# Performance work log

Measured on AMD Instinct MI355X. Metric: run time of the kernel, lower is better.

The kernel has to match this reference:

```python
import jax, jax.numpy as jnp
import numpy as np

N_NODES = 50000
N_EDGES = 800000
T = 3          # number of graph snapshots
L = 2          # num_layers
D = 128        # node feat dim == hidden dim
DE = 16        # edge feat dim


def setup_inputs() -> dict:
    key = jax.random.key(0)
    ks = jax.random.split(key, 12)
    return {
        "src": jax.random.randint(ks[0], (T, N_EDGES), 0, N_NODES, dtype=jnp.int32),
        "dst": jax.random.randint(ks[1], (T, N_EDGES), 0, N_NODES, dtype=jnp.int32),
        "n_feats": jax.random.normal(ks[2], (T, N_NODES, D), dtype=jnp.float32),
        "e_feats": jax.random.normal(ks[3], (T, N_EDGES, DE), dtype=jnp.float32),
        "W0": jax.random.normal(ks[4], (L, D, D), dtype=jnp.float32) * (1.0 / np.sqrt(D)),
        "lstm_Wih": jax.random.normal(ks[5], (L, 4 * D, D), dtype=jnp.float32) * (1.0 / np.sqrt(D)),
        "lstm_Whh": jax.random.normal(ks[6], (L, 4 * D, D), dtype=jnp.float32) * (1.0 / np.sqrt(D)),
        "lstm_bih": jnp.zeros((L, 4 * D), dtype=jnp.float32),
        "lstm_bhh": jnp.zeros((L, 4 * D), dtype=jnp.float32),
        "a_w": jax.random.normal(ks[7], (L, 2 * D + DE), dtype=jnp.float32) * 0.05,
    }


def _lstm(x, Wih, Whh, bih, bhh):
    # x: [S, H] unbatched sequence (S = D rows of W). PyTorch gate order i,f,g,o.
    H = Whh.shape[1]
    b = bih + bhh

    def step(carry, xt):
        h, c = carry
        gates = Wih @ xt + Whh @ h + b          # [4H]
        i = jax.nn.sigmoid(gates[:H])
        f = jax.nn.sigmoid(gates[H:2 * H])
        g = jnp.tanh(gates[2 * H:3 * H])
        o = jax.nn.sigmoid(gates[3 * H:])
        c = f * c + i * g
        h = o * jnp.tanh(c)
        return (h, c), h

    init = (jnp.zeros((H,), x.dtype), jnp.zeros((H,), x.dtype))
    _, hs = jax.lax.scan(step, init, x)
    return hs  # [S, H]


def _gat(src, dst, nf, ef, W, a_w, n_nodes):
    D_ = nf.shape[1]
    a_src, a_edge, a_dst = a_w[:D_], a_w[D_:D_ + ef.shape[1]], a_w[D_ + ef.shape[1]:]
    ft = nf @ W                                  # [N, H]
    s_src = nf @ a_src                           # [N]
    s_dst = nf @ a_dst                           # [N]
    score = s_src[src] + ef @ a_edge + s_dst[dst]  # [E]
    # edge softmax over destination neighborhoods
    mx = jax.ops.segment_max(score, dst, num_segments=n_nodes)
    ex = jnp.exp(score - mx[dst])
    den = jax.ops.segment_sum(ex, dst, num_segments=n_nodes)
    den = jnp.where(den == 0, 1.0, den)
    alpha = ex / den[dst]                        # [E]
    out = jax.ops.segment_sum(ft[src] * alpha[:, None], dst, num_segments=n_nodes)
    return jax.nn.leaky_relu(out)                # [N, H]


def reference(src, dst, n_feats, e_feats, W0, lstm_Wih, lstm_Whh, lstm_bih, lstm_bhh, a_w):
    n_nodes = n_feats.shape[1]
    feats = [n_feats[j] for j in range(n_feats.shape[0])]
    for i in range(W0.shape[0]):
        W = W0[i]
        for j in range(len(feats)):
            W = _lstm(W, lstm_Wih[i], lstm_Whh[i], lstm_bih[i], lstm_bhh[i])
            feats[j] = _gat(src[j], dst[j], feats[j], e_feats[j], W, a_w[i], n_nodes)
    return feats[-1]
```

## Files before the change

### kernel.cpp

```cpp
#include <hip/hip_runtime.h>
#include <cstdint>
#include <cstddef>

#define N_NODES 50000
#define N_EDGES 800000
#define D 128
#define DE 16
#define NBLK 196

__global__ void csr_hist(const int* __restrict__ dst, int* __restrict__ count){
  int e = blockIdx.x*256 + threadIdx.x;
  if (e < N_EDGES) atomicAdd(&count[dst[e]], 1);
}

__global__ __launch_bounds__(256) void csr_blocksum(const int* __restrict__ count,
                                                    int* __restrict__ bsum){
  __shared__ int red[4];
  int i = blockIdx.x*256 + threadIdx.x;
  int v = (i < N_NODES) ? count[i] : 0;
  #pragma unroll
  for (int off=32; off; off>>=1) v += __shfl_down(v, off);
  if ((threadIdx.x & 63) == 0) red[threadIdx.x>>6] = v;
  __syncthreads();
  if (threadIdx.x == 0) bsum[blockIdx.x] = red[0]+red[1]+red[2]+red[3];
}

__global__ __launch_bounds__(256) void csr_scan_bsum(const int* __restrict__ bsum,
                                                     int* __restrict__ boff){
  __shared__ int s[256];
  int t = threadIdx.x;
  int v = (t < NBLK) ? bsum[t] : 0;
  s[t] = v; __syncthreads();
  for (int off=1; off<256; off<<=1){
    int u = (t >= off) ? s[t-off] : 0;
    __syncthreads(); s[t] += u; __syncthreads();
  }
  if (t < NBLK) boff[t] = s[t] - v;
}

__global__ __launch_bounds__(256) void csr_downsweep(const int* __restrict__ count,
    const int* __restrict__ boff, int* __restrict__ row_start, int* __restrict__ cursor){
  __shared__ int s[256];
  int t = threadIdx.x;
  int i = blockIdx.x*256 + t;
  int v = (i < N_NODES) ? count[i] : 0;
  s[t] = v; __syncthreads();
  for (int off=1; off<256; off<<=1){
    int u = (t >= off) ? s[t-off] : 0;
    __syncthreads(); s[t] += u; __syncthreads();
  }
  int excl = boff[blockIdx.x] + s[t] - v;
  if (i <= N_NODES) row_start[i] = excl;
  if (i <  N_NODES) cursor[i]   = excl;
}

__global__ void csr_scatter(const int* __restrict__ src, const int* __restrict__ dst,
                            int* __restrict__ cursor, int* __restrict__ perm,
                            int* __restrict__ src_perm){
  int e = blockIdx.x*256 + threadIdx.x;
  if (e >= N_EDGES) return;
  int d = dst[e];
  int pos = atomicAdd(&cursor[d], 1);
  perm[pos] = e;
  src_perm[pos] = src[e];
}

__global__ __launch_bounds__(512) void lstm_pre(const float* __restrict__ Wih,
     const float* __restrict__ bih, const float* __restrict__ bhh,
     const float* __restrict__ xin, float* __restrict__ P){
  __shared__ float xs[128];
  int i = blockIdx.x >> 7, t = blockIdx.x & 127;
  const float* x = xin + (size_t)i*16384;
  if (threadIdx.x < 128) xs[threadIdx.x] = x[t*128 + threadIdx.x];
  __syncthreads();
  int r = threadIdx.x;
  const float4* wr = (const float4*)(Wih + (size_t)(i*512 + r)*128);
  const float4* x4 = (const float4*)xs;
  float acc = bih[i*512+r] + bhh[i*512+r];
  #pragma unroll
  for (int k=0;k<32;k++){
    float4 w = wr[k]; float4 xv = x4[k];
    acc += w.x*xv.x + w.y*xv.y + w.z*xv.z + w.w*xv.w;
  }
  P[(size_t)(i*128+t)*512 + r] = acc;
}

__global__ __launch_bounds__(512, 2) void lstm_scan(const float* __restrict__ Whh,
     const float* __restrict__ P, float* __restrict__ xout){
  __shared__ float hs[128];
  __shared__ float gs[512];
  const int i = blockIdx.x, r = threadIdx.x;
  float4 w[32];
  {
    const float4* wr = (const float4*)(Whh + (size_t)(i*512 + r)*128);
    #pragma unroll
    for (int k=0;k<32;k++) w[k] = wr[k];
  }
  float c = 0.f;
  if (r < 128) hs[r] = 0.f;
  __syncthreads();
  const float* Pi = P + (size_t)i*128*512;
  for (int t=0;t<128;t++){
    float p = Pi[t*512 + r];
    const float4* h4 = (const float4*)hs;
    float4 aA = make_float4(0.f,0.f,0.f,0.f);
    float4 aB = make_float4(0.f,0.f,0.f,0.f);
    #pragma unroll
    for (int k=0;k<32;k+=2){
      float4 ha = h4[k], hb = h4[k+1];
      float4 wa = w[k],  wb = w[k+1];
      aA.x += wa.x*ha.x; aA.y += wa.y*ha.y; aA.z += wa.z*ha.z; aA.w += wa.w*ha.w;
      aB.x += wb.x*hb.x; aB.y += wb.y*hb.y; aB.z += wb.z*hb.z; aB.w += wb.w*hb.w;
    }
    float acc = p + ((aA.x+aA.y) + (aA.z+aA.w)) + ((aB.x+aB.y) + (aB.z+aB.w));
    float g;
    if (r >= 256 && r < 384){
      float xc = fminf(fmaxf(acc, -15.f), 15.f);
      float e2 = __expf(2.f*xc);
      g = (e2 - 1.f) * __builtin_amdgcn_rcpf(e2 + 1.f);
    } else {
      g = __builtin_amdgcn_rcpf(1.f + __expf(-acc));
    }
    gs[r] = g;
    __syncthreads();
    if (r < 128){
      c = gs[128+r]*c + gs[r]*gs[256+r];
      float xc = fminf(fmaxf(c, -15.f), 15.f);
      float e2 = __expf(2.f*xc);
      float th = (e2 - 1.f) * __builtin_amdgcn_rcpf(e2 + 1.f);
      float h = gs[384+r]*th;
      hs[r] = h;
      xout[(size_t)(i*128+t)*128 + r] = h;
    }
    __syncthreads();
  }
}

__global__ __launch_bounds__(256) void gat_transform(const float* __restrict__ f,
    const float* __restrict__ W, const float* __restrict__ aw,
    float* __restrict__ ft, float* __restrict__ s_src){
  __shared__ float Ws[64*128];
  __shared__ float fs[128*36];
  int n0 = blockIdx.x * 32;
  {
    int n = threadIdx.x >> 3, kq = threadIdx.x & 7;
    int gn = n0 + n;
    #pragma unroll
    for (int p=0;p<4;p++){
      int k = kq*16 + p*4;
      float4 v = make_float4(0.f,0.f,0.f,0.f);
      if (gn < N_NODES) v = *(const float4*)(f + (size_t)gn*128 + k);
      fs[(k+0)*36+n] = v.x; fs[(k+1)*36+n] = v.y;
      fs[(k+2)*36+n] = v.z; fs[(k+3)*36+n] = v.w;
    }
  }
  int jg = threadIdx.x & 31, ng = threadIdx.x >> 5;
  float4 a0=make_float4(0,0,0,0), a1=a0, a2=a0, a3=a0;
  for (int kk=0; kk<128; kk+=64){
    __syncthreads();
    {
      const float4* W4 = (const float4*)(W + (size_t)kk*128);
      float4* Ws4w = (float4*)Ws;
      for (int idx = threadIdx.x; idx < 2048; idx += 256) Ws4w[idx] = W4[idx];
    }
    __syncthreads();
    const float4* Ws4 = (const float4*)Ws;
    #pragma unroll 4
    for (int k2=0;k2<64;k2++){
      float4 wv = Ws4[k2*32 + jg];
      float4 fv = *(const float4*)&fs[(kk+k2)*36 + (ng<<2)];
      a0.x += fv.x*wv.x; a0.y += fv.x*wv.y; a0.z += fv.x*wv.z; a0.w += fv.x*wv.w;
      a1.x += fv.y*wv.x; a1.y += fv.y*wv.y; a1.z += fv.y*wv.z; a1.w += fv.y*wv.w;
      a2.x += fv.z*wv.x; a2.y += fv.z*wv.y; a2.z += fv.z*wv.z; a2.w += fv.z*wv.w;
      a3.x += fv.w*wv.x; a3.y += fv.w*wv.y; a3.z += fv.w*wv.z; a3.w += fv.w*wv.w;
    }
  }
  int nb = n0 + (ng<<2);
  if (nb+0 < N_NODES) *(float4*)(ft + (size_t)(nb+0)*128 + (jg<<2)) = a0;
  if (nb+1 < N_NODES) *(float4*)(ft + (size_t)(nb+1)*128 + (jg<<2)) = a1;
  if (nb+2 < N_NODES) *(float4*)(ft + (size_t)(nb+2)*128 + (jg<<2)) = a2;
  if (nb+3 < N_NODES) *(float4*)(ft + (size_t)(nb+3)*128 + (jg<<2)) = a3;
  if (threadIdx.x < 32){
    int gn = n0 + threadIdx.x;
    if (gn < N_NODES){
      float s = 0.f;
      for (int k=0;k<128;k++) s += fs[k*36 + threadIdx.x] * aw[k];
      s_src[gn] = s;
    }
  }
}

__global__ __launch_bounds__(256) void gat_edge_score(const int* __restrict__ perm,
    const int* __restrict__ src_perm, const float* __restrict__ s_src,
    const float* __restrict__ ef, const float* __restrict__ aw,
    float* __restrict__ score){
  int p = blockIdx.x*256 + threadIdx.x;
  if (p >= N_EDGES) return;
  int e = perm[p];
  int s = src_perm[p];
  const float4* A = (const float4*)(aw + 128);
  float4 A0=A[0], A1=A[1], A2=A[2], A3=A[3];
  const float4* ev = (const float4*)(ef + (size_t)e*16);
  float4 v0=ev[0], v1=ev[1], v2=ev[2], v3=ev[3];
  float acc = s_src[s];
  acc += v0.x*A0.x + v0.y*A0.y + v0.z*A0.z + v0.w*A0.w;
  acc += v1.x*A1.x + v1.y*A1.y + v1.z*A1.z + v1.w*A1.w;
  acc += v2.x*A2.x + v2.y*A2.y + v2.z*A2.z + v2.w*A2.w;
  acc += v3.x*A3.x + v3.y*A3.y + v3.z*A3.z + v3.w*A3.w;
  score[p] = acc;
}

__global__ __launch_bounds__(256) void gat_aggregate(const int* __restrict__ row_start,
    const int* __restrict__ src_perm, const float* __restrict__ score,
    const float* __restrict__ ft, float* __restrict__ out){
  int lane = threadIdx.x & 63;
  int wv = threadIdx.x >> 6;
  int n = blockIdx.x*4 + wv;
  if (n >= N_NODES) return;
  int s = row_start[n], e = row_start[n+1];
  float m = -1e30f;
  for (int p = s+lane; p < e; p += 64) m = fmaxf(m, score[p]);
  #pragma unroll
  for (int off=32; off; off>>=1) m = fmaxf(m, __shfl_xor(m, off));
  float den = 0.f;
  for (int p = s+lane; p < e; p += 64) den += __expf(score[p]-m);
  #pragma unroll
  for (int off=32; off; off>>=1) den += __shfl_xor(den, off);
  float inv = (den > 0.f) ? 1.f/den : 0.f;
  float a0 = 0.f, a1 = 0.f;
  for (int p = s; p < e; p++){
    float al = __expf(score[p]-m)*inv;
    int sp = src_perm[p];
    float2 v = ((const float2*)(ft + (size_t)sp*128))[lane];
    a0 += al*v.x; a1 += al*v.y;
  }
  float2 o;
  o.x = (a0 > 0.f) ? a0 : 0.01f*a0;
  o.y = (a1 > 0.f) ? a1 : 0.01f*a1;
  ((float2*)(out + (size_t)n*128))[lane] = o;
}

extern "C" void kernel_launch(void* const* d_in, const int* in_sizes, int n_in,
                              void* d_out, int out_size, void* d_ws, size_t ws_size,
                              hipStream_t stream){
  (void)in_sizes; (void)n_in; (void)out_size; (void)ws_size;
  const int*   src     = (const int*)d_in[0] + (size_t)2*N_EDGES;
  const int*   dst     = (const int*)d_in[1] + (size_t)2*N_EDGES;
  const float* n_feats = (const float*)d_in[2] + (size_t)2*N_NODES*D;
  const float* e_feats = (const float*)d_in[3] + (size_t)2*N_EDGES*DE;
  const float* W0      = (const float*)d_in[4];
  const float* Wih     = (const float*)d_in[5];
  const float* Whh     = (const float*)d_in[6];
  const float* bih     = (const float*)d_in[7];
  const float* bhh     = (const float*)d_in[8];
  const float* a_w     = (const float*)d_in[9];
  float* out = (float*)d_out;

  char* wsp = (char*)d_ws;
  auto alloc = [&](size_t bytes)->char*{
    char* p = wsp; wsp += (bytes + 255) & ~(size_t)255; return p;
  };
  float* P         = (float*)alloc((size_t)2*128*512*4);
  float* xA        = (float*)alloc((size_t)2*128*128*4);
  float* xB        = (float*)alloc((size_t)2*128*128*4);
  int*   count     = (int*)  alloc((size_t)N_NODES*4);
  int*   bsum      = (int*)  alloc((size_t)NBLK*4);
  int*   boff      = (int*)  alloc((size_t)NBLK*4);
  int*   row_start = (int*)  alloc((size_t)(N_NODES+1)*4);
  int*   cursor    = (int*)  alloc((size_t)N_NODES*4);
  int*   perm      = (int*)  alloc((size_t)N_EDGES*4);
  int*   src_perm  = (int*)  alloc((size_t)N_EDGES*4);
  float* score     = (float*)alloc((size_t)N_EDGES*4);
  float* s_src     = (float*)alloc((size_t)N_NODES*4);
  float* ft        = (float*)alloc((size_t)N_NODES*D*4);
  float* f1        = (float*)alloc((size_t)N_NODES*D*4);

  hipMemsetAsync(count, 0, (size_t)N_NODES*4, stream);
  csr_hist     <<<(N_EDGES+255)/256, 256, 0, stream>>>(dst, count);
  csr_blocksum <<<NBLK, 256, 0, stream>>>(count, bsum);
  csr_scan_bsum<<<1,    256, 0, stream>>>(bsum, boff);
  csr_downsweep<<<NBLK, 256, 0, stream>>>(count, boff, row_start, cursor);
  csr_scatter  <<<(N_EDGES+255)/256, 256, 0, stream>>>(src, dst, cursor, perm, src_perm);

  const float* xi = W0;
  float* xo = xA;
  for (int app=0; app<3; app++){
    lstm_pre <<<256, 512, 0, stream>>>(Wih, bih, bhh, xi, P);
    lstm_scan<<<2,   512, 0, stream>>>(Whh, P, xo);
    xi = xo;
    xo = (app==0) ? xB : xA;
  }
  const float* Wfin = xA;

  const float* fin = n_feats;
  for (int l=0; l<2; l++){
    float* outl = (l==0) ? f1 : out;
    gat_transform <<<(N_NODES+31)/32, 256, 0, stream>>>(fin, Wfin + (size_t)l*16384,
                                                        a_w + (size_t)l*272, ft, s_src);
    gat_edge_score<<<(N_EDGES+255)/256, 256, 0, stream>>>(perm, src_perm, s_src,
                                                          e_feats, a_w + (size_t)l*272, score);
    gat_aggregate <<<N_NODES/4, 256, 0, stream>>>(row_start, src_perm, score, ft, outl);
    fin = f1;
  }
}
```

Measured before the change: 977.7 us.

## Interleave LSTM gate rows per hidden unit to drop a barrier; cache softmax exps

```diff
diff --git a/kernel.cpp b/kernel.cpp
--- a/kernel.cpp
+++ b/kernel.cpp
@@ -82,27 +82,33 @@
     float4 w = wr[k]; float4 xv = x4[k];
     acc += w.x*xv.x + w.y*xv.y + w.z*xv.z + w.w*xv.w;
   }
-  P[(size_t)(i*128+t)*512 + r] = acc;
+  P[(size_t)(i*128+t)*512 + (((r & 127)<<2) | (r>>7))] = acc;
 }
 
 __global__ __launch_bounds__(512, 2) void lstm_scan(const float* __restrict__ Whh,
      const float* __restrict__ P, float* __restrict__ xout){
-  __shared__ float hs[128];
-  __shared__ float gs[512];
-  const int i = blockIdx.x, r = threadIdx.x;
+  __shared__ float hs[2][128];
+  const int i = blockIdx.x;
+  const int r = threadIdx.x;
+  const int q   = r & 3;
+  const int row = r >> 2;
+  const int wr  = (q << 7) | row;
   float4 w[32];
   {
-    const float4* wr = (const float4*)(Whh + (size_t)(i*512 + r)*128);
+    const float4* wrp = (const float4*)(Whh + (size_t)(i*512 + wr)*128);
     #pragma unroll
-    for (int k=0;k<32;k++) w[k] = wr[k];
+    for (int k=0;k<32;k++) w[k] = wrp[k];
   }
   float c = 0.f;
-  if (r < 128) hs[r] = 0.f;
+  if (q == 0) hs[0][row] = 0.f;
   __syncthreads();
   const float* Pi = P + (size_t)i*128*512;
+  const bool isg = (q == 2);
+  const float kk = isg ? 2.f : 1.f;
+  int cur = 0;
   for (int t=0;t<128;t++){
     float p = Pi[t*512 + r];
-    const float4* h4 = (const float4*)hs;
+    const float4* h4 = (const float4*)hs[cur];
     float4 aA = make_float4(0.f,0.f,0.f,0.f);
     float4 aB = make_float4(0.f,0.f,0.f,0.f);
     #pragma unroll
@@ -113,26 +119,29 @@
       aB.x += wb.x*hb.x; aB.y += wb.y*hb.y; aB.z += wb.z*hb.z; aB.w += wb.w*hb.w;
     }
     float acc = p + ((aA.x+aA.y) + (aA.z+aA.w)) + ((aB.x+aB.y) + (aB.z+aB.w));
-    float g;
-    if (r >= 256 && r < 384){
-      float xc = fminf(fmaxf(acc, -15.f), 15.f);
-      float e2 = __expf(2.f*xc);
-      g = (e2 - 1.f) * __builtin_amdgcn_rcpf(e2 + 1.f);
-    } else {
-      g = __builtin_amdgcn_rcpf(1.f + __expf(-acc));
-    }
-    gs[r] = g;
+    float sg = __builtin_amdgcn_rcpf(1.f + __expf(-kk*acc));
+    float v  = isg ? (2.f*sg - 1.f) : sg;
+    float x1 = __shfl_xor(v, 1);
+    float x2 = __shfl_xor(v, 2);
+    float x3 = __shfl_xor(v, 3);
+    float t0 = (q&1)? x1 : v;
+    float t1 = (q&1)? x3 : x2;
+    float u0 = (q&1)? v  : x1;
+    float u1 = (q&1)? x2 : x3;
+    float gi = (q&2)? t1 : t0;
+    float gf = (q&2)? u1 : u0;
+    float gg = (q&2)? t0 : t1;
+    float go = (q&2)? u0 : u1;
+    c = gf*c + gi*gg;
+    float xc = fminf(fmaxf(c, -15.f), 15.f);
+    float e2 = __expf(2.f*xc);
+    float th = (e2 - 1.f) * __builtin_amdgcn_rcpf(e2 + 1.f);
+    float h  = go * th;
+    int nxt = cur ^ 1;
+    if (q == 0) hs[nxt][row] = h;
     __syncthreads();
-    if (r < 128){
-      c = gs[128+r]*c + gs[r]*gs[256+r];
-      float xc = fminf(fmaxf(c, -15.f), 15.f);
-      float e2 = __expf(2.f*xc);
-      float th = (e2 - 1.f) * __builtin_amdgcn_rcpf(e2 + 1.f);
-      float h = gs[384+r]*th;
-      hs[r] = h;
-      xout[(size_t)(i*128+t)*128 + r] = h;
-    }
-    __syncthreads();
+    if (q == 0) xout[(size_t)(i*128+t)*128 + row] = h;
+    cur = nxt;
   }
 }
 
@@ -211,7 +220,7 @@
 }
 
 __global__ __launch_bounds__(256) void gat_aggregate(const int* __restrict__ row_start,
-    const int* __restrict__ src_perm, const float* __restrict__ score,
+    const int* __restrict__ src_perm, float* __restrict__ score,
     const float* __restrict__ ft, float* __restrict__ out){
   int lane = threadIdx.x & 63;
   int wv = threadIdx.x >> 6;
@@ -223,13 +232,17 @@
   #pragma unroll
   for (int off=32; off; off>>=1) m = fmaxf(m, __shfl_xor(m, off));
   float den = 0.f;
-  for (int p = s+lane; p < e; p += 64) den += __expf(score[p]-m);
+  for (int p = s+lane; p < e; p += 64){
+    float ex = __expf(score[p]-m);
+    den += ex;
+    score[p] = ex;
+  }
   #pragma unroll
   for (int off=32; off; off>>=1) den += __shfl_xor(den, off);
   float inv = (den > 0.f) ? 1.f/den : 0.f;
   float a0 = 0.f, a1 = 0.f;
   for (int p = s; p < e; p++){
-    float al = __expf(score[p]-m)*inv;
+    float al = score[p]*inv;
     int sp = src_perm[p];
     float2 v = ((const float2*)(ft + (size_t)sp*128))[lane];
     a0 += al*v.x; a1 += al*v.y;
```

After: 1.095 ms. 1.12x slower.

## Split LSTM recurrence matvec across K-chunks and cache softmax exponentials in aggregate

Applied to the files above, without the earlier changes.

```diff
diff --git a/kernel.cpp b/kernel.cpp
--- a/kernel.cpp
+++ b/kernel.cpp
@@ -88,51 +88,78 @@
 __global__ __launch_bounds__(512, 2) void lstm_scan(const float* __restrict__ Whh,
      const float* __restrict__ P, float* __restrict__ xout){
   __shared__ float hs[128];
-  __shared__ float gs[512];
-  const int i = blockIdx.x, r = threadIdx.x;
-  float4 w[32];
+  __shared__ float part[4][512];
+  const int i  = blockIdx.x;
+  const int r  = threadIdx.x;
+  const int w  = r >> 6;
+  const int l  = r & 63;
+  const int kc = w >> 1;
+  const int rh = w & 1;
+  const int row0 = rh*256 + l*4;
+  float4 wv[4][8];
   {
-    const float4* wr = (const float4*)(Whh + (size_t)(i*512 + r)*128);
+    const float* base = Whh + (size_t)i*512*128 + (size_t)row0*128 + kc*32;
     #pragma unroll
-    for (int k=0;k<32;k++) w[k] = wr[k];
+    for (int ri=0; ri<4; ri++){
+      const float4* p4 = (const float4*)(base + ri*128);
+      #pragma unroll
+      for (int j=0;j<8;j++) wv[ri][j] = p4[j];
+    }
   }
   float c = 0.f;
+  float hreg = 0.f;
   if (r < 128) hs[r] = 0.f;
   __syncthreads();
   const float* Pi = P + (size_t)i*128*512;
-  for (int t=0;t<128;t++){
-    float p = Pi[t*512 + r];
-    const float4* h4 = (const float4*)hs;
-    float4 aA = make_float4(0.f,0.f,0.f,0.f);
-    float4 aB = make_float4(0.f,0.f,0.f,0.f);
+  float* xo = xout + (size_t)i*128*128;
+  for (int t=0; t<128; t++){
+    float p0=0.f, p1=0.f, p2=0.f, p3=0.f;
+    if (r < 128){
+      p0 = Pi[t*512 +   0 + r];
+      p1 = Pi[t*512 + 128 + r];
+      p2 = Pi[t*512 + 256 + r];
+      p3 = Pi[t*512 + 384 + r];
+    }
+    const float4* h4 = ((const float4*)hs) + kc*8;
+    float4 a0 = make_float4(0.f,0.f,0.f,0.f);
+    float4 a1 = a0, a2 = a0, a3 = a0;
     #pragma unroll
-    for (int k=0;k<32;k+=2){
-      float4 ha = h4[k], hb = h4[k+1];
-      float4 wa = w[k],  wb = w[k+1];
-      aA.x += wa.x*ha.x; aA.y += wa.y*ha.y; aA.z += wa.z*ha.z; aA.w += wa.w*ha.w;
-      aB.x += wb.x*hb.x; aB.y += wb.y*hb.y; aB.z += wb.z*hb.z; aB.w += wb.w*hb.w;
-    }
-    float acc = p + ((aA.x+aA.y) + (aA.z+aA.w)) + ((aB.x+aB.y) + (aB.z+aB.w));
-    float g;
-    if (r >= 256 && r < 384){
-      float xc = fminf(fmaxf(acc, -15.f), 15.f);
-      float e2 = __expf(2.f*xc);
-      g = (e2 - 1.f) * __builtin_amdgcn_rcpf(e2 + 1.f);
-    } else {
-      g = __builtin_amdgcn_rcpf(1.f + __expf(-acc));
-    }
-    gs[r] = g;
+    for (int j=0;j<8;j++){
+      float4 hv = h4[j];
+      float4 w0 = wv[0][j], w1 = wv[1][j], w2 = wv[2][j], w3 = wv[3][j];
+      a0.x += w0.x*hv.x; a0.y += w0.y*hv.y; a0.z += w0.z*hv.z; a0.w += w0.w*hv.w;
+      a1.x += w1.x*hv.x; a1.y += w1.y*hv.y; a1.z += w1.z*hv.z; a1.w += w1.w*hv.w;
+      a2.x += w2.x*hv.x; a2.y += w2.y*hv.y; a2.z += w2.z*hv.z; a2.w += w2.w*hv.w;
+      a3.x += w3.x*hv.x; a3.y += w3.y*hv.y; a3.z += w3.z*hv.z; a3.w += w3.w*hv.w;
+    }
+    float4 pr;
+    pr.x = (a0.x+a0.y) + (a0.z+a0.w);
+    pr.y = (a1.x+a1.y) + (a1.z+a1.w);
+    pr.z = (a2.x+a2.y) + (a2.z+a2.w);
+    pr.w = (a3.x+a3.y) + (a3.z+a3.w);
+    *(float4*)&part[kc][row0] = pr;
     __syncthreads();
     if (r < 128){
-      c = gs[128+r]*c + gs[r]*gs[256+r];
+      int j = r;
+      float s0 = ((part[0][      j] + part[1][      j]) + (part[2][      j] + part[3][      j])) + p0;
+      float s1 = ((part[0][128 + j] + part[1][128 + j]) + (part[2][128 + j] + part[3][128 + j])) + p1;
+      float s2 = ((part[0][256 + j] + part[1][256 + j]) + (part[2][256 + j] + part[3][256 + j])) + p2;
+      float s3 = ((part[0][384 + j] + part[1][384 + j]) + (part[2][384 + j] + part[3][384 + j])) + p3;
+      float gi = __builtin_amdgcn_rcpf(1.f + __expf(-s0));
+      float gf = __builtin_amdgcn_rcpf(1.f + __expf(-s1));
+      float xg = fminf(fmaxf(s2, -15.f), 15.f);
+      float eg = __expf(2.f*xg);
+      float gg = (eg - 1.f) * __builtin_amdgcn_rcpf(eg + 1.f);
+      float go = __builtin_amdgcn_rcpf(1.f + __expf(-s3));
+      c = gf*c + gi*gg;
       float xc = fminf(fmaxf(c, -15.f), 15.f);
       float e2 = __expf(2.f*xc);
       float th = (e2 - 1.f) * __builtin_amdgcn_rcpf(e2 + 1.f);
-      float h = gs[384+r]*th;
-      hs[r] = h;
-      xout[(size_t)(i*128+t)*128 + r] = h;
+      hreg = go*th;
+      hs[j] = hreg;
     }
     __syncthreads();
+    if (r < 128) xo[t*128 + r] = hreg;
   }
 }
 
@@ -211,7 +238,7 @@
 }
 
 __global__ __launch_bounds__(256) void gat_aggregate(const int* __restrict__ row_start,
-    const int* __restrict__ src_perm, const float* __restrict__ score,
+    const int* __restrict__ src_perm, float* __restrict__ score,
     const float* __restrict__ ft, float* __restrict__ out){
   int lane = threadIdx.x & 63;
   int wv = threadIdx.x >> 6;
@@ -223,13 +250,17 @@
   #pragma unroll
   for (int off=32; off; off>>=1) m = fmaxf(m, __shfl_xor(m, off));
   float den = 0.f;
-  for (int p = s+lane; p < e; p += 64) den += __expf(score[p]-m);
+  for (int p = s+lane; p < e; p += 64){
+    float ex = __expf(score[p]-m);
+    den += ex;
+    score[p] = ex;
+  }
   #pragma unroll
   for (int off=32; off; off>>=1) den += __shfl_xor(den, off);
   float inv = (den > 0.f) ? 1.f/den : 0.f;
   float a0 = 0.f, a1 = 0.f;
   for (int p = s; p < e; p++){
-    float al = __expf(score[p]-m)*inv;
+    float al = score[p]*inv;
     int sp = src_perm[p];
     float2 v = ((const float2*)(ft + (size_t)sp*128))[lane];
     a0 += al*v.x; a1 += al*v.y;
```

Result: faster. 937.5 us (-4.1%).
